# Optimization experiments

Measured on AMD Instinct MI355X. Metric: run time of the kernel, lower is better.

## Reference

```python
import jax, jax.numpy as jnp
import numpy as np

SCALE = 64 ** 0.5  # module hard-codes sqrt(64), independent of output_dim


def setup_inputs() -> dict:
    key = jax.random.key(0)
    kx, kw = jax.random.split(key)
    x = jax.random.normal(kx, (8, 2048, 768), dtype=jnp.float32)
    kernel = jax.random.normal(kw, (3, 768, 768), dtype=jnp.float32) * 0.02
    return {"x": x, "kernel": kernel}


def reference(x, kernel):
    # x: [b, s, d]; kernel: [3, d, o]
    q = jnp.einsum('bsd,do->bso', x, kernel[0])
    k = jnp.einsum('bsd,do->bso', x, kernel[1])
    v = jnp.einsum('bsd,do->bso', x, kernel[2])
    scores = jnp.einsum('bso,bto->bst', q, k) / SCALE  # [b, s, s]
    attn = jax.nn.softmax(scores, axis=-1)
    return jnp.einsum('bst,bto->bso', attn, v)
```

## Files before the change

### kernel.cpp

```cpp
#include <hip/hip_runtime.h>

typedef unsigned short u16;
typedef unsigned int   u32;
typedef unsigned long long u64;
typedef __bf16  bf16x8 __attribute__((ext_vector_type(8)));
typedef float   f32x4  __attribute__((ext_vector_type(4)));

__device__ __forceinline__ u16 f2bf(float f) {
  u32 u = __builtin_bit_cast(u32, f);
  u += 0x7FFFu + ((u >> 16) & 1u);
  return (u16)(u >> 16);
}
__device__ __forceinline__ u32 pack2(float lo, float hi) {
  return (u32)f2bf(lo) | ((u32)f2bf(hi) << 16);
}

__device__ __forceinline__ void gload_lds16(const u16* g, u16* l) {
  __builtin_amdgcn_global_load_lds((const __attribute__((address_space(1))) void*)g,
                                   (__attribute__((address_space(3))) void*)l,
                                   16, 0, 0);
}

__global__ __launch_bounds__(256) void prep(const float* __restrict__ x,
                                            const float* __restrict__ w,
                                            u16* __restrict__ Xb,
                                            u16* __restrict__ Wt) {
  if (blockIdx.z < 3) {
    if (blockIdx.x >= 12 || blockIdx.y >= 12) return;
    __shared__ u16 t[64][65];
    const float* iz = w + (size_t)blockIdx.z * 768 * 768;
    u16* oz = Wt + (size_t)blockIdx.z * 768 * 768;
    const int tx = threadIdx.x & 63, ty = threadIdx.x >> 6;
    const int r0 = blockIdx.y * 64, c0 = blockIdx.x * 64;
#pragma unroll
    for (int rr = ty; rr < 64; rr += 4)
      t[rr][tx] = f2bf(iz[(size_t)(r0 + rr) * 768 + c0 + tx]);
    __syncthreads();
#pragma unroll
    for (int rr = ty; rr < 64; rr += 4)
      oz[(size_t)(c0 + rr) * 768 + r0 + tx] = t[tx][rr];
  } else {
    const size_t lin = (size_t)(blockIdx.z - 3) * 256 + blockIdx.y * 16 + blockIdx.x;
    const size_t i = lin * 256 + threadIdx.x;
    const float4* in4 = (const float4*)x;
    float4 a = in4[2 * i], b = in4[2 * i + 1];
    uint4 o;
    o.x = pack2(a.x, a.y); o.y = pack2(a.z, a.w);
    o.z = pack2(b.x, b.y); o.w = pack2(b.z, b.w);
    ((uint4*)Xb)[i] = o;
  }
}

template <int MODE, typename CT>
__global__ __launch_bounds__(256, 2)
void gemm_bt(const u16* __restrict__ A, const u16* __restrict__ B,
             CT* __restrict__ C, int Kd, int lda, int ldb, int ldc,
             size_t strideA, size_t strideB, size_t strideC,
             float* __restrict__ lsum, u16* __restrict__ vtp) {
  __shared__ __align__(16) u16 sh[2][128 * 64];
  u16* sA = sh[0];
  u16* sB = sh[1];

  const u32 gx = gridDim.x, gy = gridDim.y;
  const u32 lin = blockIdx.x + gx * (blockIdx.y + gy * blockIdx.z);
  const u32 nblk = gx * gy * gridDim.z;
  const u32 newlin = (lin & 7u) * (nblk >> 3) + (lin >> 3);
  const u32 bx = newlin % gx;
  const u32 tmp = newlin / gx;
  const u32 by = tmp % gy;
  const u32 bz = tmp / gy;

  const u16* Az = A + (size_t)bz * strideA;
  const u16* Bz = B + (size_t)bz * strideB;
  const int m0 = by * 128;
  int n0 = bx * 128;
  int matrix = 0;
  CT* Cz;
  if (MODE == 3) {
    matrix = n0 / 768;
    Cz = C + (size_t)matrix * strideC;
    n0 = n0 % 768;
  } else {
    Cz = C + (size_t)bz * strideC;
  }

  const int tid = threadIdx.x;
  const int lane = tid & 63, wave = tid >> 6;
  const int wm = (wave >> 1) * 64, wn = (wave & 1) * 64;
  const int lr = lane & 15, quad = lane >> 4;

  const u16* gA = Az + (size_t)(by * 128) * lda;
  const u16* gB = Bz + (size_t)(bx * 128) * ldb;
  const int stRow = wave * 8 + (lane >> 3);
  const int stCol = ((lane & 7) ^ (lane >> 3)) << 3;

  f32x4 acc[4][4] = {};

  for (int k0 = 0; k0 < Kd; k0 += 64) {
#pragma unroll
    for (int r = 0; r < 4; ++r) {
      gload_lds16(gA + (size_t)(stRow + r * 32) * lda + (k0 + stCol),
                  (u16*)((char*)sA + r * 4096 + wave * 1024));
      gload_lds16(gB + (size_t)(stRow + r * 32) * ldb + (k0 + stCol),
                  (u16*)((char*)sB + r * 4096 + wave * 1024));
    }
    __syncthreads();
#pragma unroll
    for (int kc = 0; kc < 2; ++kc) {
      bf16x8 af[4], bfv[4];
      const int coff = (((kc << 2) + quad) ^ (lr & 7)) << 4;
#pragma unroll
      for (int t = 0; t < 4; ++t) {
        af[t]  = *(const bf16x8*)((const char*)sA + (wm + t * 16 + lr) * 128 + coff);
        bfv[t] = *(const bf16x8*)((const char*)sB + (wn + t * 16 + lr) * 128 + coff);
      }
#pragma unroll
      for (int mt = 0; mt < 4; ++mt)
#pragma unroll
        for (int nt = 0; nt < 4; ++nt)
          acc[mt][nt] = __builtin_amdgcn_mfma_f32_16x16x32_bf16(
              af[mt], bfv[nt], acc[mt][nt], 0, 0, 0);
    }
    __syncthreads();
  }

  if (MODE == 1) {
    float* rowsum = (float*)sA;
    if (tid < 128) rowsum[tid] = 0.f;
    __syncthreads();
#pragma unroll
    for (int mt = 0; mt < 4; ++mt) {
#pragma unroll
      for (int i = 0; i < 4; ++i) {
        const int row_l = wm + mt * 16 + quad * 4 + i;
        CT* cp = Cz + (size_t)(m0 + row_l) * ldc + (n0 + wn + lr);
        float e[4], s = 0.f;
#pragma unroll
        for (int nt = 0; nt < 4; ++nt) {
          e[nt] = __expf(acc[mt][nt][i] * 0.125f);
          s += e[nt];
          cp[nt * 16] = f2bf(e[nt]);
        }
        s += __shfl_xor(s, 1);  s += __shfl_xor(s, 2);
        s += __shfl_xor(s, 4);  s += __shfl_xor(s, 8);
        if (lr == 0) atomicAdd(&rowsum[row_l], s);
      }
    }
    __syncthreads();
    if (tid < 128)
      lsum[(size_t)bx * 16384 + (size_t)bz * 2048 + m0 + tid] = rowsum[tid];
  } else if (MODE == 2) {
    float* rinv = (float*)sA;
    if (tid < 128) {
      float s = 0.f;
      const size_t base = (size_t)bz * 2048 + m0 + tid;
#pragma unroll
      for (int xt = 0; xt < 16; ++xt) s += lsum[(size_t)xt * 16384 + base];
      rinv[tid] = 1.0f / s;
    }
    __syncthreads();
#pragma unroll
    for (int mt = 0; mt < 4; ++mt) {
#pragma unroll
      for (int i = 0; i < 4; ++i) {
        const int row_l = wm + mt * 16 + quad * 4 + i;
        const float iv = rinv[row_l];
        CT* cp = Cz + (size_t)(m0 + row_l) * ldc + (n0 + wn + lr);
#pragma unroll
        for (int nt = 0; nt < 4; ++nt) cp[nt * 16] = acc[mt][nt][i] * iv;
      }
    }
  } else if (MODE == 3 && matrix == 2) {
    u16* T = sh[0];
#pragma unroll
    for (int mt = 0; mt < 4; ++mt) {
      const int rg = (wave >> 1) * 16 + mt * 4 + quad;
#pragma unroll
      for (int nt = 0; nt < 4; ++nt) {
        const int col = wn + nt * 16 + lr;
        u64 v = (u64)f2bf(acc[mt][nt][0])
              | ((u64)f2bf(acc[mt][nt][1]) << 16)
              | ((u64)f2bf(acc[mt][nt][2]) << 32)
              | ((u64)f2bf(acc[mt][nt][3]) << 48);
        *(u64*)((char*)T + col * 256 + ((rg ^ (col & 31)) << 3)) = v;
      }
    }
    __syncthreads();
    const int b = m0 >> 11;
    const int t0 = (m0 & 2047) + (lane << 1);
    const int n0v = n0;
#pragma unroll
    for (int it = 0; it < 32; ++it) {
      const int col = it * 4 + wave;
      const u32 val = *(const u32*)((char*)T + col * 256 +
                                    (((lane >> 1) ^ (col & 31)) << 3) +
                                    ((lane & 1) << 2));
      *(u32*)(vtp + ((size_t)b * 768 + n0v + col) * 2048 + t0) = val;
    }
  } else {
#pragma unroll
    for (int mt = 0; mt < 4; ++mt) {
#pragma unroll
      for (int i = 0; i < 4; ++i) {
        const int row_l = wm + mt * 16 + quad * 4 + i;
        CT* cp = Cz + (size_t)(m0 + row_l) * ldc + (n0 + wn + lr);
#pragma unroll
        for (int nt = 0; nt < 4; ++nt) cp[nt * 16] = f2bf(acc[mt][nt][i]);
      }
    }
  }
}

extern "C" void kernel_launch(void* const* d_in, const int* in_sizes, int n_in,
                              void* d_out, int out_size, void* d_ws, size_t ws_size,
                              hipStream_t stream) {
  const float* x = (const float*)d_in[0];
  const float* w = (const float*)d_in[1];
  float* out = (float*)d_out;
  char* ws = (char*)d_ws;

  const size_t NS = (size_t)16384 * 768;
  u16* Sc = (u16*)ws;
  u16* Xb = (u16*)ws;
  u16* Wt = (u16*)(ws + NS * 2);
  u16* Qm = (u16*)(ws + 67108864);
  u16* Km = Qm + NS;
  float* Lpart = (float*)(ws + 117440512);
  u16* Vt = (u16*)(ws + 142606336);

  prep<<<dim3(16, 16, 27), 256, 0, stream>>>(x, w, Xb, Wt);
  gemm_bt<3, u16><<<dim3(18, 128, 1), 256, 0, stream>>>(
      Xb, Wt, Qm, 768, 768, 768, 768, (size_t)0, (size_t)0, NS, Lpart, Vt);
  gemm_bt<1, u16><<<dim3(16, 16, 8), 256, 0, stream>>>(
      Qm, Km, Sc, 768, 768, 768, 2048, (size_t)2048 * 768, (size_t)2048 * 768,
      (size_t)2048 * 2048, Lpart, nullptr);
  gemm_bt<2, float><<<dim3(6, 16, 8), 256, 0, stream>>>(
      Sc, Vt, out, 2048, 2048, 2048, 768, (size_t)2048 * 2048,
      (size_t)768 * 2048, (size_t)2048 * 768, Lpart, nullptr);
}
```

Baseline: 279.8 us.

## Use 256x256 tiles with 8 waves and double-buffered LDS pipelined GEMM

Moves the GEMM kernel from 128x128 tiles with 4 waves to 256x256 tiles with 8 waves and double-buffered LDS. The next K tile's global-to-LDS load is issued while the current one is computed, and MFMA phases are split across barriers with s_setprio. This is meant to raise arithmetic intensity and hide load latency behind the MFMA work. In exchange it uses 128KB of LDS per block and more registers, and it leaves fewer blocks for small grids (for example 3x8x8 in the final GEMM), which could hurt occupancy and wave fill.

```diff
diff --git a/kernel.cpp b/kernel.cpp
--- a/kernel.cpp
+++ b/kernel.cpp
@@ -52,14 +52,12 @@
 }
 
 template <int MODE, typename CT>
-__global__ __launch_bounds__(256, 2)
+__global__ __launch_bounds__(512, 2)
 void gemm_bt(const u16* __restrict__ A, const u16* __restrict__ B,
              CT* __restrict__ C, int Kd, int lda, int ldb, int ldc,
              size_t strideA, size_t strideB, size_t strideC,
              float* __restrict__ lsum, u16* __restrict__ vtp) {
-  __shared__ __align__(16) u16 sh[2][128 * 64];
-  u16* sA = sh[0];
-  u16* sB = sh[1];
+  __shared__ __align__(16) u16 sh[2][2][256 * 64];
 
   const u32 gx = gridDim.x, gy = gridDim.y;
   const u32 lin = blockIdx.x + gx * (blockIdx.y + gy * blockIdx.z);
@@ -72,64 +70,95 @@
 
   const u16* Az = A + (size_t)bz * strideA;
   const u16* Bz = B + (size_t)bz * strideB;
-  const int m0 = by * 128;
-  int n0 = bx * 128;
+  const int m0 = by * 256;
+  const int n0g = bx * 256;
+  int n0 = n0g;
   int matrix = 0;
   CT* Cz;
   if (MODE == 3) {
-    matrix = n0 / 768;
+    matrix = n0g / 768;
     Cz = C + (size_t)matrix * strideC;
-    n0 = n0 % 768;
+    n0 = n0g % 768;
   } else {
     Cz = C + (size_t)bz * strideC;
   }
 
   const int tid = threadIdx.x;
   const int lane = tid & 63, wave = tid >> 6;
-  const int wm = (wave >> 1) * 64, wn = (wave & 1) * 64;
+  const int wr = wave >> 2, wc = wave & 3;
+  const int wm = wr * 128, wn = wc * 64;
   const int lr = lane & 15, quad = lane >> 4;
-
-  const u16* gA = Az + (size_t)(by * 128) * lda;
-  const u16* gB = Bz + (size_t)(bx * 128) * ldb;
-  const int stRow = wave * 8 + (lane >> 3);
-  const int stCol = ((lane & 7) ^ (lane >> 3)) << 3;
-
-  f32x4 acc[4][4] = {};
-
-  for (int k0 = 0; k0 < Kd; k0 += 64) {
+  const int sr = lane >> 3;
+  const int sc = ((lane & 7) ^ sr) << 3;
+
+  const u16* gA = Az + (size_t)m0 * lda;
+  const u16* gB = Bz + (size_t)n0g * ldb;
+
+  f32x4 acc[8][4] = {};
+  const int NT = Kd >> 6;
+
+  auto stage = [&](int buf, int k0) {
 #pragma unroll
     for (int r = 0; r < 4; ++r) {
-      gload_lds16(gA + (size_t)(stRow + r * 32) * lda + (k0 + stCol),
-                  (u16*)((char*)sA + r * 4096 + wave * 1024));
-      gload_lds16(gB + (size_t)(stRow + r * 32) * ldb + (k0 + stCol),
-                  (u16*)((char*)sB + r * 4096 + wave * 1024));
-    }
-    __syncthreads();
-#pragma unroll
-    for (int kc = 0; kc < 2; ++kc) {
-      bf16x8 af[4], bfv[4];
-      const int coff = (((kc << 2) + quad) ^ (lr & 7)) << 4;
-#pragma unroll
-      for (int t = 0; t < 4; ++t) {
-        af[t]  = *(const bf16x8*)((const char*)sA + (wm + t * 16 + lr) * 128 + coff);
-        bfv[t] = *(const bf16x8*)((const char*)sB + (wn + t * 16 + lr) * 128 + coff);
-      }
-#pragma unroll
-      for (int mt = 0; mt < 4; ++mt)
+      const int rows = r * 64 + wave * 8;
+      gload_lds16(gA + (size_t)(rows + sr) * lda + (k0 + sc), &sh[buf][0][rows * 64]);
+      gload_lds16(gB + (size_t)(rows + sr) * ldb + (k0 + sc), &sh[buf][1][rows * 64]);
+    }
+  };
+
+  stage(0, 0);
+  asm volatile("s_waitcnt vmcnt(0)" ::: "memory");
+  __builtin_amdgcn_s_barrier();
+
+  for (int t = 0; t < NT; ++t) {
+    const char* sAc = (const char*)sh[t & 1][0];
+    const char* sBc = (const char*)sh[t & 1][1];
+    bf16x8 bq[4][2];
+#pragma unroll
+    for (int p = 0; p < 4; ++p) {
+      if (p == 0 && t + 1 < NT) stage((t + 1) & 1, (t + 1) << 6);
+      bf16x8 aq[2][2];
+#pragma unroll
+      for (int mi = 0; mi < 2; ++mi)
+#pragma unroll
+        for (int kc = 0; kc < 2; ++kc)
+          aq[mi][kc] = *(const bf16x8*)(sAc + (wm + (2 * p + mi) * 16 + lr) * 128 +
+                                        ((((kc << 2) + quad) ^ (lr & 7)) << 4));
+      if (p == 0) {
 #pragma unroll
         for (int nt = 0; nt < 4; ++nt)
-          acc[mt][nt] = __builtin_amdgcn_mfma_f32_16x16x32_bf16(
-              af[mt], bfv[nt], acc[mt][nt], 0, 0, 0);
-    }
-    __syncthreads();
+#pragma unroll
+          for (int kc = 0; kc < 2; ++kc)
+            bq[nt][kc] = *(const bf16x8*)(sBc + (wn + nt * 16 + lr) * 128 +
+                                          ((((kc << 2) + quad) ^ (lr & 7)) << 4));
+      }
+      asm volatile("" ::: "memory");
+      __builtin_amdgcn_s_barrier();
+      asm volatile("s_waitcnt lgkmcnt(0)" ::: "memory");
+      __builtin_amdgcn_sched_barrier(0);
+      __builtin_amdgcn_s_setprio(1);
+#pragma unroll
+      for (int mi = 0; mi < 2; ++mi)
+#pragma unroll
+        for (int nt = 0; nt < 4; ++nt)
+#pragma unroll
+          for (int kc = 0; kc < 2; ++kc)
+            acc[2 * p + mi][nt] = __builtin_amdgcn_mfma_f32_16x16x32_bf16(
+                aq[mi][kc], bq[nt][kc], acc[2 * p + mi][nt], 0, 0, 0);
+      __builtin_amdgcn_s_setprio(0);
+      asm volatile("" ::: "memory");
+      if (p < 3) __builtin_amdgcn_s_barrier();
+    }
+    asm volatile("s_waitcnt vmcnt(0)" ::: "memory");
+    __builtin_amdgcn_s_barrier();
   }
 
   if (MODE == 1) {
-    float* rowsum = (float*)sA;
-    if (tid < 128) rowsum[tid] = 0.f;
-    __syncthreads();
-#pragma unroll
-    for (int mt = 0; mt < 4; ++mt) {
+    float* rowsum = (float*)sh;
+    if (tid < 256) rowsum[tid] = 0.f;
+    __syncthreads();
+#pragma unroll
+    for (int mt = 0; mt < 8; ++mt) {
 #pragma unroll
       for (int i = 0; i < 4; ++i) {
         const int row_l = wm + mt * 16 + quad * 4 + i;
@@ -147,20 +176,20 @@
       }
     }
     __syncthreads();
-    if (tid < 128)
+    if (tid < 256)
       lsum[(size_t)bx * 16384 + (size_t)bz * 2048 + m0 + tid] = rowsum[tid];
   } else if (MODE == 2) {
-    float* rinv = (float*)sA;
-    if (tid < 128) {
+    float* rinv = (float*)sh;
+    if (tid < 256) {
       float s = 0.f;
       const size_t base = (size_t)bz * 2048 + m0 + tid;
 #pragma unroll
-      for (int xt = 0; xt < 16; ++xt) s += lsum[(size_t)xt * 16384 + base];
+      for (int xt = 0; xt < 8; ++xt) s += lsum[(size_t)xt * 16384 + base];
       rinv[tid] = 1.0f / s;
     }
     __syncthreads();
 #pragma unroll
-    for (int mt = 0; mt < 4; ++mt) {
+    for (int mt = 0; mt < 8; ++mt) {
 #pragma unroll
       for (int i = 0; i < 4; ++i) {
         const int row_l = wm + mt * 16 + quad * 4 + i;
@@ -171,10 +200,10 @@
       }
     }
   } else if (MODE == 3 && matrix == 2) {
-    u16* T = sh[0];
-#pragma unroll
-    for (int mt = 0; mt < 4; ++mt) {
-      const int rg = (wave >> 1) * 16 + mt * 4 + quad;
+    u16* T = &sh[0][0][0];
+#pragma unroll
+    for (int mt = 0; mt < 8; ++mt) {
+      const int rg = wr * 32 + mt * 4 + quad;
 #pragma unroll
       for (int nt = 0; nt < 4; ++nt) {
         const int col = wn + nt * 16 + lr;
@@ -182,24 +211,26 @@
               | ((u64)f2bf(acc[mt][nt][1]) << 16)
               | ((u64)f2bf(acc[mt][nt][2]) << 32)
               | ((u64)f2bf(acc[mt][nt][3]) << 48);
-        *(u64*)((char*)T + col * 256 + ((rg ^ (col & 31)) << 3)) = v;
+        *(u64*)((char*)T + col * 512 + ((rg ^ (col & 63)) << 3)) = v;
       }
     }
     __syncthreads();
     const int b = m0 >> 11;
-    const int t0 = (m0 & 2047) + (lane << 1);
-    const int n0v = n0;
-#pragma unroll
+#pragma unroll 4
     for (int it = 0; it < 32; ++it) {
-      const int col = it * 4 + wave;
-      const u32 val = *(const u32*)((char*)T + col * 256 +
-                                    (((lane >> 1) ^ (col & 31)) << 3) +
-                                    ((lane & 1) << 2));
-      *(u32*)(vtp + ((size_t)b * 768 + n0v + col) * 2048 + t0) = val;
+      const int col = it * 8 + wave;
+#pragma unroll
+      for (int h = 0; h < 2; ++h) {
+        const int rg = h * 32 + (lane >> 1);
+        const u32 val = *(const u32*)((const char*)T + col * 512 +
+                                      ((rg ^ (col & 63)) << 3) + ((lane & 1) << 2));
+        *(u32*)(vtp + ((size_t)b * 768 + n0 + col) * 2048 +
+                (m0 & 2047) + h * 128 + (lane << 1)) = val;
+      }
     }
   } else {
 #pragma unroll
-    for (int mt = 0; mt < 4; ++mt) {
+    for (int mt = 0; mt < 8; ++mt) {
 #pragma unroll
       for (int i = 0; i < 4; ++i) {
         const int row_l = wm + mt * 16 + quad * 4 + i;
@@ -224,17 +255,16 @@
   u16* Xb = (u16*)ws;
   u16* Wt = (u16*)(ws + NS * 2);
   u16* Qm = (u16*)(ws + 67108864);
-  u16* Km = Qm + NS;
   float* Lpart = (float*)(ws + 117440512);
   u16* Vt = (u16*)(ws + 142606336);
 
   prep<<<dim3(16, 16, 27), 256, 0, stream>>>(x, w, Xb, Wt);
-  gemm_bt<3, u16><<<dim3(18, 128, 1), 256, 0, stream>>>(
+  gemm_bt<3, u16><<<dim3(9, 64, 1), 512, 0, stream>>>(
       Xb, Wt, Qm, 768, 768, 768, 768, (size_t)0, (size_t)0, NS, Lpart, Vt);
-  gemm_bt<1, u16><<<dim3(16, 16, 8), 256, 0, stream>>>(
-      Qm, Km, Sc, 768, 768, 768, 2048, (size_t)2048 * 768, (size_t)2048 * 768,
+  gemm_bt<1, u16><<<dim3(8, 8, 8), 512, 0, stream>>>(
+      Qm, Qm + NS, Sc, 768, 768, 768, 2048, (size_t)2048 * 768, (size_t)2048 * 768,
       (size_t)2048 * 2048, Lpart, nullptr);
-  gemm_bt<2, float><<<dim3(6, 16, 8), 256, 0, stream>>>(
+  gemm_bt<2, float><<<dim3(3, 8, 8), 512, 0, stream>>>(
       Sc, Vt, out, 2048, 2048, 2048, 768, (size_t)2048 * 2048,
       (size_t)768 * 2048, (size_t)2048 * 768, Lpart, nullptr);
 }
```

After: 305.8 us. +9.3%, slower.
